# Kernel tuning notes

Measured on AMD Instinct MI355X. Metric: run time of the kernel, lower is better.

Reference implementation:

```python
import jax, jax.numpy as jnp
import numpy as np

EMBED = 512
HEADS = 1
HEAD_DIM = EMBED // HEADS  # 512 (heads must be 1 for the original torch code to run)
N, S = 4, 4096


def setup_inputs() -> dict:
    key = jax.random.key(0)
    ks = jax.random.split(key, 9)
    scale = 1.0 / np.sqrt(EMBED)
    return {
        "values": jax.random.normal(ks[0], (N, 1, S, EMBED), dtype=jnp.float32),
        "keys": jax.random.normal(ks[1], (N, 1, S, EMBED), dtype=jnp.float32),
        "query": jax.random.normal(ks[2], (N, 1, S, EMBED), dtype=jnp.float32),
        "mask": jax.random.randint(ks[3], (N, 1, S, S), 0, 2, dtype=jnp.int32),
        "Wv": jax.random.normal(ks[4], (EMBED, EMBED), dtype=jnp.float32) * scale,
        "Wk": jax.random.normal(ks[5], (EMBED, EMBED), dtype=jnp.float32) * scale,
        "Wq": jax.random.normal(ks[6], (EMBED, EMBED), dtype=jnp.float32) * scale,
        "Wo": jax.random.normal(ks[7], (EMBED, EMBED), dtype=jnp.float32) * scale,
        "bo": jnp.zeros((EMBED,), dtype=jnp.float32),
    }


def reference(values, keys, query, mask, Wv, Wk, Wq, Wo, bo):
    n = query.shape[0]
    q_len = query.shape[2]
    # reshape(N, -1, heads, head_dim); inputs are [N, 1, S, E] -> [N, S, H, Dh]
    v = values.reshape(n, -1, HEADS, HEAD_DIM)
    k = keys.reshape(n, -1, HEADS, HEAD_DIM)
    q = query.reshape(n, -1, HEADS, HEAD_DIM)
    # per-module linear projections (nn.Linear: y = x @ W.T)
    v = jnp.einsum('nlhd,ed->nlhe', v, Wv)
    k = jnp.einsum('nlhd,ed->nlhe', k, Wk)
    q = jnp.einsum('nqhd,ed->nqhe', q, Wq)
    # full [N, H, Q, K] score matrix, as in the original
    energy = jnp.einsum('nqhd,nkhd->nhqk', q, k)
    energy = jnp.where(mask == 0, jnp.float32(-1e20), energy)
    attn = jax.nn.softmax(energy / np.sqrt(HEAD_DIM), axis=3)
    out = jnp.einsum('nhql,nlhd->nqhd', attn, v).reshape(n, q_len, HEADS * HEAD_DIM)
    return out @ Wo.T + bo
```

## Files before the change

### kernel.cpp

```cpp
#include <hip/hip_runtime.h>

typedef __bf16 bf16x8 __attribute__((ext_vector_type(8)));
typedef __bf16 bf16x4 __attribute__((ext_vector_type(4)));
typedef float f32x4 __attribute__((ext_vector_type(4)));
typedef float f32x16 __attribute__((ext_vector_type(16)));

#define MFMA16(a, b, c) __builtin_amdgcn_mfma_f32_16x16x32_bf16((a), (b), (c), 0, 0, 0)
#define MFMA32(a, b, c) __builtin_amdgcn_mfma_f32_32x32x16_bf16((a), (b), (c), 0, 0, 0)

static constexpr int SEQ = 4096;
static constexpr int DIM = 512;

typedef __attribute__((address_space(3))) void lds_void;
typedef __attribute__((address_space(1))) const void gbl_void;

__device__ __forceinline__ void glds16(const void* g, void* l) {
    __builtin_amdgcn_global_load_lds((gbl_void*)g, (lds_void*)l, 16, 0, 0);
}

__device__ __forceinline__ bf16x8 cvt8f(const float* __restrict__ p) {
    float4 f0 = *(const float4*)p;
    float4 f1 = *(const float4*)(p + 4);
    bf16x8 v;
    v[0] = (__bf16)f0.x; v[1] = (__bf16)f0.y; v[2] = (__bf16)f0.z; v[3] = (__bf16)f0.w;
    v[4] = (__bf16)f1.x; v[5] = (__bf16)f1.y; v[6] = (__bf16)f1.z; v[7] = (__bf16)f1.w;
    return v;
}

__global__ __launch_bounds__(256)
void convert_w(const float* __restrict__ wq, const float* __restrict__ wk,
               const float* __restrict__ wv, const float* __restrict__ wo,
               __bf16* __restrict__ out)
{
    const int z = blockIdx.y;
    const float* src = (z == 0) ? wq : (z == 1) ? wk : (z == 2) ? wv : wo;
    __bf16* dst = out + (size_t)z * DIM * DIM;
    const int i = (blockIdx.x * 256 + threadIdx.x) * 8;
    *(bf16x8*)(dst + i) = cvt8f(src + i);
}

__global__ __launch_bounds__(256, 3)
void gemm_qkv(const float* __restrict__ Aq, const float* __restrict__ Ak,
              const float* __restrict__ Av, const __bf16* __restrict__ Wb,
              __bf16* __restrict__ Qp, __bf16* __restrict__ Kp,
              __bf16* __restrict__ Vtp)
{
    const int z = blockIdx.z;
    const float* Ap = (z == 0) ? Aq : (z == 1) ? Ak : Av;
    const __bf16* Bp = Wb + (size_t)z * DIM * DIM;
    __bf16* Cp = (z == 0) ? Qp : (z == 1) ? Kp : Vtp;

    __shared__ __align__(16) char smem[128 * 132 * 2];
    __bf16* As = (__bf16*)smem;
    __bf16* Bs = (__bf16*)(smem + 16384);

    const int tid  = threadIdx.x;
    const int wave = tid >> 6;
    const int lane = tid & 63;
    const int quad = lane >> 4;
    const int l16  = lane & 15;
    const int m0 = blockIdx.x * 128;
    const int n0 = blockIdx.y * 128;
    const int wm = (wave >> 1) * 64;
    const int wn = (wave & 1) * 64;

    f32x4 acc[4][4] = {};

    for (int k0 = 0; k0 < DIM; k0 += 64) {
        #pragma unroll
        for (int i = 0; i < 4; i++) {
            const int j = wave * 4 + i;
            const int t = j * 64 + lane;
            const int row = t >> 3, c8 = t & 7;
            glds16(Bp + (size_t)(n0 + row) * DIM + k0 + c8 * 8, &Bs[j * 512]);
            *(bf16x8*)&As[t * 8] =
                cvt8f(Ap + (size_t)(m0 + row) * DIM + k0 + c8 * 8);
        }
        __syncthreads();
        #pragma unroll
        for (int kk = 0; kk < 2; kk++) {
            bf16x8 af[4], bg[4];
            #pragma unroll
            for (int mt = 0; mt < 4; mt++)
                af[mt] = *(const bf16x8*)&As[(wm + mt * 16 + l16) * 64 + kk * 32 + quad * 8];
            #pragma unroll
            for (int nt = 0; nt < 4; nt++)
                bg[nt] = *(const bf16x8*)&Bs[(wn + nt * 16 + l16) * 64 + kk * 32 + quad * 8];
            #pragma unroll
            for (int mt = 0; mt < 4; mt++)
                #pragma unroll
                for (int nt = 0; nt < 4; nt++)
                    acc[mt][nt] = MFMA16(af[mt], bg[nt], acc[mt][nt]);
        }
        __syncthreads();
    }

    if (z < 2) {
        #pragma unroll
        for (int mt = 0; mt < 4; mt++)
            #pragma unroll
            for (int nt = 0; nt < 4; nt++)
                #pragma unroll
                for (int r = 0; r < 4; r++)
                    Cp[(size_t)(m0 + wm + mt * 16 + quad * 4 + r) * DIM
                       + n0 + wn + nt * 16 + l16] = (__bf16)acc[mt][nt][r];
    } else {
        __bf16* Tt = (__bf16*)smem;
        __syncthreads();
        #pragma unroll
        for (int mt = 0; mt < 4; mt++)
            #pragma unroll
            for (int nt = 0; nt < 4; nt++)
                #pragma unroll
                for (int r = 0; r < 4; r++)
                    Tt[(wm + mt * 16 + quad * 4 + r) * 132 + wn + nt * 16 + l16]
                        = (__bf16)acc[mt][nt][r];
        __syncthreads();
        const int nb  = m0 >> 12;
        const int s0m = m0 & 4095;
        const int d   = tid >> 1;
        const int sh  = (tid & 1) * 64;
        __bf16* dst = Cp + (size_t)nb * DIM * SEQ + (size_t)(n0 + d) * SEQ + s0m + sh;
        #pragma unroll
        for (int i = 0; i < 8; i++) {
            bf16x8 vv;
            #pragma unroll
            for (int e = 0; e < 8; e++) vv[e] = Tt[(sh + i * 8 + e) * 132 + d];
            *(bf16x8*)(dst + i * 8) = vv;
        }
    }
}

__global__ __launch_bounds__(256, 3)
void gemm_out(const __bf16* __restrict__ Ap, const __bf16* __restrict__ Bp,
              float* __restrict__ Cp, const float* __restrict__ bias)
{
    __shared__ __align__(16) __bf16 As[128 * 64];
    __shared__ __align__(16) __bf16 Bs[128 * 64];
    const int tid  = threadIdx.x;
    const int wave = tid >> 6;
    const int lane = tid & 63;
    const int quad = lane >> 4;
    const int l16  = lane & 15;
    const int m0 = blockIdx.x * 128;
    const int n0 = blockIdx.y * 128;
    const int wm = (wave >> 1) * 64;
    const int wn = (wave & 1) * 64;

    f32x4 acc[4][4] = {};

    for (int k0 = 0; k0 < DIM; k0 += 64) {
        #pragma unroll
        for (int i = 0; i < 4; i++) {
            const int j = wave * 4 + i;
            const int c = j * 64 + lane;
            const int row = c >> 3, c8 = c & 7;
            glds16(Ap + (size_t)(m0 + row) * DIM + k0 + c8 * 8, &As[j * 512]);
            glds16(Bp + (size_t)(n0 + row) * DIM + k0 + c8 * 8, &Bs[j * 512]);
        }
        __syncthreads();
        #pragma unroll
        for (int kk = 0; kk < 2; kk++) {
            bf16x8 af[4], bg[4];
            #pragma unroll
            for (int mt = 0; mt < 4; mt++)
                af[mt] = *(const bf16x8*)&As[(wm + mt * 16 + l16) * 64 + kk * 32 + quad * 8];
            #pragma unroll
            for (int nt = 0; nt < 4; nt++)
                bg[nt] = *(const bf16x8*)&Bs[(wn + nt * 16 + l16) * 64 + kk * 32 + quad * 8];
            #pragma unroll
            for (int mt = 0; mt < 4; mt++)
                #pragma unroll
                for (int nt = 0; nt < 4; nt++)
                    acc[mt][nt] = MFMA16(af[mt], bg[nt], acc[mt][nt]);
        }
        __syncthreads();
    }
    #pragma unroll
    for (int mt = 0; mt < 4; mt++)
        #pragma unroll
        for (int nt = 0; nt < 4; nt++)
            #pragma unroll
            for (int r = 0; r < 4; r++) {
                const int col = n0 + wn + nt * 16 + l16;
                Cp[(size_t)(m0 + wm + mt * 16 + quad * 4 + r) * DIM + col]
                    = acc[mt][nt][r] + bias[col];
            }
}

#define MKC(v, r4) ((r4) == 0 ? (v).x : (r4) == 1 ? (v).y : (r4) == 2 ? (v).z : (v).w)
#define WAITLGKM() asm volatile("s_waitcnt lgkmcnt(0)" ::: "memory")
#define BARRIER()  asm volatile("s_barrier" ::: "memory")

__global__ __launch_bounds__(512, 1)
void flash_attn(__bf16* __restrict__ Qp, const __bf16* __restrict__ Kp,
                const __bf16* __restrict__ Vt, const int* __restrict__ mask)
{
    constexpr float SCALE = 0.044194173824159216f;
    constexpr int QPITCH = 520;
    constexpr int PPITCH = 264;

    __shared__ __align__(16) __bf16 Qs[64 * QPITCH];
    __shared__ __align__(16) __bf16 P[64 * PPITCH];
    __shared__ float pmax[8 * 66];
    __shared__ float psum[8 * 66];

    const int bid  = blockIdx.x;
    const int n    = bid & 3;
    const int q0   = (bid >> 2) * 64;
    const int tid  = threadIdx.x;
    const int w    = tid >> 6;
    const int lane = tid & 63;
    const int l32  = lane & 31;
    const int half = lane >> 5;

    const __bf16* Qb = Qp + (size_t)n * SEQ * DIM;
    const __bf16* Kb = Kp + (size_t)n * SEQ * DIM;
    const __bf16* Vb = Vt + (size_t)n * DIM * SEQ;
    const int*    Mb = mask + (size_t)n * SEQ * SEQ;
    __bf16*       AO = Qp + (size_t)n * SEQ * DIM;

    #pragma unroll
    for (int i = 0; i < 8; i++) {
        const int r = i * 8 + w;
        glds16(Qb + (size_t)(q0 + r) * DIM + lane * 8, &Qs[r * QPITCH]);
    }

    const __bf16* kPtr  = Kb + (size_t)(32 * w + l32) * DIM + half * 8;
    const __bf16* vPtr0 = Vb + (size_t)(32 * w + l32) * SEQ + half * 8;
    const __bf16* vPtr1 = vPtr0 + (size_t)256 * SEQ;

    const int qrow0 = l32 * QPITCH;
    const int qrow1 = (32 + l32) * QPITCH;

    float m0 = -__builtin_inff(), m1 = -__builtin_inff();
    float l0 = 0.f, l1 = 0.f;
    f32x16 o00 = {}, o01 = {}, o10 = {}, o11 = {};
    f32x16 s0, s1;

    bf16x8 kA[4], kB[4], kC[4], vA[4], vB[4], vC[4];

#define LOADKB(buf, base, dc_) { _Pragma("unroll") \
    for (int ks = 0; ks < 4; ks++) \
        buf[ks] = *(const bf16x8*)((base) + (dc_) * 64 + ks * 16); }

#define LOADV(buf, vc_) { const __bf16* vp_ = ((vc_) < 4) ? vPtr0 : vPtr1; \
    _Pragma("unroll") \
    for (int ks = 0; ks < 4; ks++) \
        buf[ks] = *(const bf16x8*)(vp_ + ((vc_) & 3) * 64 + ks * 16); }

#define QK8(buf, dc_) { __builtin_amdgcn_s_setprio(1); \
    _Pragma("unroll") \
    for (int ks = 0; ks < 4; ks++) { \
        bf16x8 b0 = *(const bf16x8*)&Qs[qrow0 + (dc_) * 64 + (2 * ks + half) * 8]; \
        bf16x8 b1 = *(const bf16x8*)&Qs[qrow1 + (dc_) * 64 + (2 * ks + half) * 8]; \
        s0 = MFMA32(buf[ks], b0, s0); \
        s1 = MFMA32(buf[ks], b1, s1); \
    } __builtin_amdgcn_s_setprio(0); }

#define PV8(buf, vc_) { __builtin_amdgcn_s_setprio(1); \
    _Pragma("unroll") \
    for (int ks = 0; ks < 4; ks++) { \
        const int ck = ((vc_) & 3) * 8 + 2 * ks + half; \
        bf16x8 b0 = *(const bf16x8*)&P[l32 * PPITCH + ck * 8]; \
        bf16x8 b1 = *(const bf16x8*)&P[(32 + l32) * PPITCH + ck * 8]; \
        if ((vc_) < 4) { o00 = MFMA32(buf[ks], b0, o00); o01 = MFMA32(buf[ks], b1, o01); } \
        else           { o10 = MFMA32(buf[ks], b0, o10); o11 = MFMA32(buf[ks], b1, o11); } \
    } __builtin_amdgcn_s_setprio(0); }

    __syncthreads();
    LOADKB(kA, kPtr, 0);
    LOADKB(kB, kPtr, 1);

    #pragma unroll 1
    for (int j = 0; j < 16; j++) {
        const int k0 = j * 256;

        int4 mk0[4], mk1[4];
        {
            const int* mp0 = Mb + (size_t)(q0 + l32) * SEQ + k0 + 32 * w + 4 * half;
            const int* mp1 = mp0 + (size_t)32 * SEQ;
            #pragma unroll
            for (int g = 0; g < 4; g++) {
                mk0[g] = *(const int4*)(mp0 + 8 * g);
                mk1[g] = *(const int4*)(mp1 + 8 * g);
            }
        }

        s0 = (f32x16){}; s1 = (f32x16){};
        LOADKB(kC, kPtr, 2);
        QK8(kA, 0); LOADKB(kA, kPtr, 3);
        QK8(kB, 1); LOADKB(kB, kPtr, 4);
        QK8(kC, 2); LOADKB(kC, kPtr, 5);
        QK8(kA, 3); LOADKB(kA, kPtr, 6);
        QK8(kB, 4); LOADKB(kB, kPtr, 7);
        QK8(kC, 5); LOADV(vA, 0);
        QK8(kA, 6); LOADV(vB, 1);
        QK8(kB, 7); LOADV(vC, 2);

        {
            float mx0 = s0[0], mx1 = s1[0];
            #pragma unroll
            for (int r = 1; r < 16; r++) { mx0 = fmaxf(mx0, s0[r]); mx1 = fmaxf(mx1, s1[r]); }
            mx0 = fmaxf(mx0, __shfl_xor(mx0, 32));
            mx1 = fmaxf(mx1, __shfl_xor(mx1, 32));
            if (half == 0) pmax[w * 66 + l32]      = mx0;
            else           pmax[w * 66 + 32 + l32] = mx1;
        }
        WAITLGKM();
        BARRIER();

        float mp0v = pmax[l32], mp1v = pmax[32 + l32];
        #pragma unroll
        for (int w2 = 1; w2 < 8; w2++) {
            mp0v = fmaxf(mp0v, pmax[w2 * 66 + l32]);
            mp1v = fmaxf(mp1v, pmax[w2 * 66 + 32 + l32]);
        }
        const float mn0 = fmaxf(m0, mp0v * SCALE);
        const float mn1 = fmaxf(m1, mp1v * SCALE);
        const float a0 = __expf(m0 - mn0);
        const float a1 = __expf(m1 - mn1);
        m0 = mn0; m1 = mn1;
        #pragma unroll
        for (int r = 0; r < 16; r++) {
            o00[r] *= a0; o10[r] *= a0;
            o01[r] *= a1; o11[r] *= a1;
        }

        float ls0 = 0.f, ls1 = 0.f;
        #pragma unroll
        for (int g = 0; g < 4; g++) {
            bf16x4 pv0, pv1;
            #pragma unroll
            for (int r4 = 0; r4 < 4; r4++) {
                const int r = g * 4 + r4;
                float p0 = __expf(s0[r] * SCALE - mn0);
                float p1 = __expf(s1[r] * SCALE - mn1);
                p0 = MKC(mk0[g], r4) ? p0 : 0.f;
                p1 = MKC(mk1[g], r4) ? p1 : 0.f;
                ls0 += p0; ls1 += p1;
                pv0[r4] = (__bf16)p0;
                pv1[r4] = (__bf16)p1;
            }
            const int c = 4 * w + g;
            *(bf16x4*)&P[l32 * PPITCH + c * 8 + 4 * half]        = pv0;
            *(bf16x4*)&P[(32 + l32) * PPITCH + c * 8 + 4 * half] = pv1;
        }
        ls0 += __shfl_xor(ls0, 32);
        ls1 += __shfl_xor(ls1, 32);
        if (half == 0) psum[w * 66 + l32]      = ls0;
        else           psum[w * 66 + 32 + l32] = ls1;
        WAITLGKM();
        BARRIER();

        {
            float ss0 = 0.f, ss1 = 0.f;
            #pragma unroll
            for (int w2 = 0; w2 < 8; w2++) {
                ss0 += psum[w2 * 66 + l32];
                ss1 += psum[w2 * 66 + 32 + l32];
            }
            l0 = l0 * a0 + ss0;
            l1 = l1 * a1 + ss1;
        }

        PV8(vA, 0); LOADV(vA, 3);
        PV8(vB, 1); LOADV(vB, 4);
        PV8(vC, 2); LOADV(vC, 5);
        PV8(vA, 3); LOADV(vA, 6);
        PV8(vB, 4); LOADV(vB, 7);
        PV8(vC, 5); if (j < 15) LOADKB(kA, kPtr + 256 * DIM, 0);
        PV8(vA, 6); if (j < 15) LOADKB(kB, kPtr + 256 * DIM, 1);
        PV8(vB, 7);

        kPtr  += 256 * DIM;
        vPtr0 += 256;
        vPtr1 += 256;
        WAITLGKM();
        BARRIER();
    }

    const float li0 = 1.f / l0, li1 = 1.f / l1;
    __bf16* ao0 = AO + (size_t)(q0 + l32) * DIM;
    __bf16* ao1 = AO + (size_t)(q0 + 32 + l32) * DIM;
    #pragma unroll
    for (int h = 0; h < 2; h++) {
        #pragma unroll
        for (int g = 0; g < 4; g++) {
            bf16x4 v00, v01;
            #pragma unroll
            for (int r4 = 0; r4 < 4; r4++) {
                const int r = g * 4 + r4;
                v00[r4] = (__bf16)((h ? o10[r] : o00[r]) * li0);
                v01[r4] = (__bf16)((h ? o11[r] : o01[r]) * li1);
            }
            const int d = h * 256 + 32 * w + g * 8 + 4 * half;
            *(bf16x4*)&ao0[d] = v00;
            *(bf16x4*)&ao1[d] = v01;
        }
    }
#undef LOADKB
#undef LOADV
#undef QK8
#undef PV8
}

extern "C" void kernel_launch(void* const* d_in, const int* in_sizes, int n_in,
                              void* d_out, int out_size, void* d_ws, size_t ws_size,
                              hipStream_t stream)
{
    const float* values = (const float*)d_in[0];
    const float* keys   = (const float*)d_in[1];
    const float* query  = (const float*)d_in[2];
    const int*   mask   = (const int*)d_in[3];
    const float* Wv = (const float*)d_in[4];
    const float* Wk = (const float*)d_in[5];
    const float* Wq = (const float*)d_in[6];
    const float* Wo = (const float*)d_in[7];
    const float* bo = (const float*)d_in[8];
    float* out = (float*)d_out;

    char* ws = (char*)d_ws;
    __bf16* Qp  = (__bf16*)(ws);
    __bf16* Kp  = (__bf16*)(ws + (16u << 20));
    __bf16* Vt  = (__bf16*)(ws + (32u << 20));
    __bf16* wbf = (__bf16*)(ws + (48u << 20));

    const int M = 4 * SEQ;

    convert_w<<<dim3(128, 4), 256, 0, stream>>>(Wq, Wk, Wv, Wo, wbf);

    gemm_qkv<<<dim3(M / 128, DIM / 128, 3), 256, 0, stream>>>(
        query, keys, values, wbf, Qp, Kp, Vt);

    flash_attn<<<256, 512, 0, stream>>>(Qp, Kp, Vt, mask);

    gemm_out<<<dim3(M / 128, DIM / 128), 256, 0, stream>>>(
        Qp , wbf + 3 * DIM * DIM, out, bo);
}
```

Before: 724.2 us.

## Halve flash-attention query tile to 32 rows and run two blocks per CU

Shrinks each flash_attn block from 64 to 32 query rows, doubling the grid to 512 blocks and setting launch bounds to allow two blocks per CU. Accumulators, score registers and the K/V register buffers are cut (triple to double buffering), which lowers register and LDS pressure so more waves can hide latency. In exchange every K and V tile is loaded from memory twice as often per query row, and the MFMA-to-load ratio per wave drops.

```diff
diff --git a/kernel.cpp b/kernel.cpp
--- a/kernel.cpp
+++ b/kernel.cpp
@@ -192,7 +192,7 @@
 #define WAITLGKM() asm volatile("s_waitcnt lgkmcnt(0)" ::: "memory")
 #define BARRIER()  asm volatile("s_barrier" ::: "memory")
 
-__global__ __launch_bounds__(512, 1)
+__global__ __launch_bounds__(512, 2)
 void flash_attn(__bf16* __restrict__ Qp, const __bf16* __restrict__ Kp,
                 const __bf16* __restrict__ Vt, const int* __restrict__ mask)
 {
@@ -200,14 +200,14 @@
     constexpr int QPITCH = 520;
     constexpr int PPITCH = 264;
 
-    __shared__ __align__(16) __bf16 Qs[64 * QPITCH];
-    __shared__ __align__(16) __bf16 P[64 * PPITCH];
-    __shared__ float pmax[8 * 66];
-    __shared__ float psum[8 * 66];
+    __shared__ __align__(16) __bf16 Qs[32 * QPITCH];
+    __shared__ __align__(16) __bf16 P[32 * PPITCH];
+    __shared__ float pmax[8 * 33];
+    __shared__ float psum[8 * 33];
 
     const int bid  = blockIdx.x;
     const int n    = bid & 3;
-    const int q0   = (bid >> 2) * 64;
+    const int q0   = (bid >> 2) * 32;
     const int tid  = threadIdx.x;
     const int w    = tid >> 6;
     const int lane = tid & 63;
@@ -221,7 +221,7 @@
     __bf16*       AO = Qp + (size_t)n * SEQ * DIM;
 
     #pragma unroll
-    for (int i = 0; i < 8; i++) {
+    for (int i = 0; i < 4; i++) {
         const int r = i * 8 + w;
         glds16(Qb + (size_t)(q0 + r) * DIM + lane * 8, &Qs[r * QPITCH]);
     }
@@ -231,14 +231,13 @@
     const __bf16* vPtr1 = vPtr0 + (size_t)256 * SEQ;
 
     const int qrow0 = l32 * QPITCH;
-    const int qrow1 = (32 + l32) * QPITCH;
-
-    float m0 = -__builtin_inff(), m1 = -__builtin_inff();
-    float l0 = 0.f, l1 = 0.f;
-    f32x16 o00 = {}, o01 = {}, o10 = {}, o11 = {};
-    f32x16 s0, s1;
-
-    bf16x8 kA[4], kB[4], kC[4], vA[4], vB[4], vC[4];
+
+    float m0 = -__builtin_inff();
+    float l0 = 0.f;
+    f32x16 o00 = {}, o10 = {};
+    f32x16 s0;
+
+    bf16x8 kA[4], kB[4], vA[4], vB[4];
 
 #define LOADKB(buf, base, dc_) { _Pragma("unroll") \
     for (int ks = 0; ks < 4; ks++) \
@@ -253,9 +252,7 @@
     _Pragma("unroll") \
     for (int ks = 0; ks < 4; ks++) { \
         bf16x8 b0 = *(const bf16x8*)&Qs[qrow0 + (dc_) * 64 + (2 * ks + half) * 8]; \
-        bf16x8 b1 = *(const bf16x8*)&Qs[qrow1 + (dc_) * 64 + (2 * ks + half) * 8]; \
         s0 = MFMA32(buf[ks], b0, s0); \
-        s1 = MFMA32(buf[ks], b1, s1); \
     } __builtin_amdgcn_s_setprio(0); }
 
 #define PV8(buf, vc_) { __builtin_amdgcn_s_setprio(1); \
@@ -263,9 +260,8 @@
     for (int ks = 0; ks < 4; ks++) { \
         const int ck = ((vc_) & 3) * 8 + 2 * ks + half; \
         bf16x8 b0 = *(const bf16x8*)&P[l32 * PPITCH + ck * 8]; \
-        bf16x8 b1 = *(const bf16x8*)&P[(32 + l32) * PPITCH + ck * 8]; \
-        if ((vc_) < 4) { o00 = MFMA32(buf[ks], b0, o00); o01 = MFMA32(buf[ks], b1, o01); } \
-        else           { o10 = MFMA32(buf[ks], b0, o10); o11 = MFMA32(buf[ks], b1, o11); } \
+        if ((vc_) < 4) { o00 = MFMA32(buf[ks], b0, o00); } \
+        else           { o10 = MFMA32(buf[ks], b0, o10); } \
     } __builtin_amdgcn_s_setprio(0); }
 
     __syncthreads();
@@ -276,102 +272,77 @@
     for (int j = 0; j < 16; j++) {
         const int k0 = j * 256;
 
-        int4 mk0[4], mk1[4];
+        int4 mk0[4];
         {
             const int* mp0 = Mb + (size_t)(q0 + l32) * SEQ + k0 + 32 * w + 4 * half;
-            const int* mp1 = mp0 + (size_t)32 * SEQ;
-            #pragma unroll
-            for (int g = 0; g < 4; g++) {
-                mk0[g] = *(const int4*)(mp0 + 8 * g);
-                mk1[g] = *(const int4*)(mp1 + 8 * g);
-            }
-        }
-
-        s0 = (f32x16){}; s1 = (f32x16){};
-        LOADKB(kC, kPtr, 2);
-        QK8(kA, 0); LOADKB(kA, kPtr, 3);
-        QK8(kB, 1); LOADKB(kB, kPtr, 4);
-        QK8(kC, 2); LOADKB(kC, kPtr, 5);
-        QK8(kA, 3); LOADKB(kA, kPtr, 6);
-        QK8(kB, 4); LOADKB(kB, kPtr, 7);
-        QK8(kC, 5); LOADV(vA, 0);
-        QK8(kA, 6); LOADV(vB, 1);
-        QK8(kB, 7); LOADV(vC, 2);
+            #pragma unroll
+            for (int g = 0; g < 4; g++) mk0[g] = *(const int4*)(mp0 + 8 * g);
+        }
+
+        s0 = (f32x16){};
+        QK8(kA, 0); LOADKB(kA, kPtr, 2);
+        QK8(kB, 1); LOADKB(kB, kPtr, 3);
+        QK8(kA, 2); LOADKB(kA, kPtr, 4);
+        QK8(kB, 3); LOADKB(kB, kPtr, 5);
+        QK8(kA, 4); LOADKB(kA, kPtr, 6);
+        QK8(kB, 5); LOADKB(kB, kPtr, 7);
+        QK8(kA, 6); LOADV(vA, 0);
+        QK8(kB, 7); LOADV(vB, 1);
 
         {
-            float mx0 = s0[0], mx1 = s1[0];
-            #pragma unroll
-            for (int r = 1; r < 16; r++) { mx0 = fmaxf(mx0, s0[r]); mx1 = fmaxf(mx1, s1[r]); }
+            float mx0 = s0[0];
+            #pragma unroll
+            for (int r = 1; r < 16; r++) mx0 = fmaxf(mx0, s0[r]);
             mx0 = fmaxf(mx0, __shfl_xor(mx0, 32));
-            mx1 = fmaxf(mx1, __shfl_xor(mx1, 32));
-            if (half == 0) pmax[w * 66 + l32]      = mx0;
-            else           pmax[w * 66 + 32 + l32] = mx1;
+            if (half == 0) pmax[w * 33 + l32] = mx0;
         }
         WAITLGKM();
         BARRIER();
 
-        float mp0v = pmax[l32], mp1v = pmax[32 + l32];
-        #pragma unroll
-        for (int w2 = 1; w2 < 8; w2++) {
-            mp0v = fmaxf(mp0v, pmax[w2 * 66 + l32]);
-            mp1v = fmaxf(mp1v, pmax[w2 * 66 + 32 + l32]);
-        }
+        float mp0v = pmax[l32];
+        #pragma unroll
+        for (int w2 = 1; w2 < 8; w2++) mp0v = fmaxf(mp0v, pmax[w2 * 33 + l32]);
         const float mn0 = fmaxf(m0, mp0v * SCALE);
-        const float mn1 = fmaxf(m1, mp1v * SCALE);
         const float a0 = __expf(m0 - mn0);
-        const float a1 = __expf(m1 - mn1);
-        m0 = mn0; m1 = mn1;
-        #pragma unroll
-        for (int r = 0; r < 16; r++) {
-            o00[r] *= a0; o10[r] *= a0;
-            o01[r] *= a1; o11[r] *= a1;
-        }
-
-        float ls0 = 0.f, ls1 = 0.f;
+        m0 = mn0;
+        #pragma unroll
+        for (int r = 0; r < 16; r++) { o00[r] *= a0; o10[r] *= a0; }
+
+        float ls0 = 0.f;
         #pragma unroll
         for (int g = 0; g < 4; g++) {
-            bf16x4 pv0, pv1;
+            bf16x4 pv0;
             #pragma unroll
             for (int r4 = 0; r4 < 4; r4++) {
                 const int r = g * 4 + r4;
                 float p0 = __expf(s0[r] * SCALE - mn0);
-                float p1 = __expf(s1[r] * SCALE - mn1);
                 p0 = MKC(mk0[g], r4) ? p0 : 0.f;
-                p1 = MKC(mk1[g], r4) ? p1 : 0.f;
-                ls0 += p0; ls1 += p1;
+                ls0 += p0;
                 pv0[r4] = (__bf16)p0;
-                pv1[r4] = (__bf16)p1;
             }
             const int c = 4 * w + g;
-            *(bf16x4*)&P[l32 * PPITCH + c * 8 + 4 * half]        = pv0;
-            *(bf16x4*)&P[(32 + l32) * PPITCH + c * 8 + 4 * half] = pv1;
+            *(bf16x4*)&P[l32 * PPITCH + c * 8 + 4 * half] = pv0;
         }
         ls0 += __shfl_xor(ls0, 32);
-        ls1 += __shfl_xor(ls1, 32);
-        if (half == 0) psum[w * 66 + l32]      = ls0;
-        else           psum[w * 66 + 32 + l32] = ls1;
+        if (half == 0) psum[w * 33 + l32] = ls0;
         WAITLGKM();
         BARRIER();
 
         {
-            float ss0 = 0.f, ss1 = 0.f;
-            #pragma unroll
-            for (int w2 = 0; w2 < 8; w2++) {
-                ss0 += psum[w2 * 66 + l32];
-                ss1 += psum[w2 * 66 + 32 + l32];
-            }
+            float ss0 = 0.f;
+            #pragma unroll
+            for (int w2 = 0; w2 < 8; w2++) ss0 += psum[w2 * 33 + l32];
             l0 = l0 * a0 + ss0;
-            l1 = l1 * a1 + ss1;
-        }
-
-        PV8(vA, 0); LOADV(vA, 3);
-        PV8(vB, 1); LOADV(vB, 4);
-        PV8(vC, 2); LOADV(vC, 5);
-        PV8(vA, 3); LOADV(vA, 6);
-        PV8(vB, 4); LOADV(vB, 7);
-        PV8(vC, 5); if (j < 15) LOADKB(kA, kPtr + 256 * DIM, 0);
-        PV8(vA, 6); if (j < 15) LOADKB(kB, kPtr + 256 * DIM, 1);
-        PV8(vB, 7);
+        }
+
+        PV8(vA, 0); LOADV(vA, 2);
+        PV8(vB, 1); LOADV(vB, 3);
+        PV8(vA, 2); LOADV(vA, 4);
+        PV8(vB, 3); LOADV(vB, 5);
+        PV8(vA, 4); LOADV(vA, 6);
+        PV8(vB, 5); LOADV(vB, 7);
+        PV8(vA, 6); if (j < 15) LOADKB(kA, kPtr + 256 * DIM, 0);
+        PV8(vB, 7); if (j < 15) LOADKB(kB, kPtr + 256 * DIM, 1);
 
         kPtr  += 256 * DIM;
         vPtr0 += 256;
@@ -380,23 +351,20 @@
         BARRIER();
     }
 
-    const float li0 = 1.f / l0, li1 = 1.f / l1;
+    const float li0 = 1.f / l0;
     __bf16* ao0 = AO + (size_t)(q0 + l32) * DIM;
-    __bf16* ao1 = AO + (size_t)(q0 + 32 + l32) * DIM;
     #pragma unroll
     for (int h = 0; h < 2; h++) {
         #pragma unroll
         for (int g = 0; g < 4; g++) {
-            bf16x4 v00, v01;
+            bf16x4 v00;
             #pragma unroll
             for (int r4 = 0; r4 < 4; r4++) {
                 const int r = g * 4 + r4;
                 v00[r4] = (__bf16)((h ? o10[r] : o00[r]) * li0);
-                v01[r4] = (__bf16)((h ? o11[r] : o01[r]) * li1);
             }
             const int d = h * 256 + 32 * w + g * 8 + 4 * half;
             *(bf16x4*)&ao0[d] = v00;
-            *(bf16x4*)&ao1[d] = v01;
         }
     }
 #undef LOADKB
@@ -433,7 +401,7 @@
     gemm_qkv<<<dim3(M / 128, DIM / 128, 3), 256, 0, stream>>>(
         query, keys, values, wbf, Qp, Kp, Vt);
 
-    flash_attn<<<256, 512, 0, stream>>>(Qp, Kp, Vt, mask);
+    flash_attn<<<512, 512, 0, stream>>>(Qp, Kp, Vt, mask);
 
     gemm_out<<<dim3(M / 128, DIM / 128), 256, 0, stream>>>(
         Qp , wbf + 3 * DIM * DIM, out, bo);
```

Result: slower. 930.3 us (+28.4%).
